# Kernel optimization log

Hardware: AMD Instinct MI355X
Metric: run time of the kernel (lower is better)

Reference implementation:

```python
import jax, jax.numpy as jnp
import numpy as np

ALPHA = 0.1
NUM_CLASSES = 10000
FEAT_DIM = 256
BATCH = 8192


def setup_inputs() -> dict:
    key = jax.random.key(0)
    k1, k2, k3 = jax.random.split(key, 3)
    feat = jax.random.normal(k1, (BATCH, FEAT_DIM), dtype=jnp.float32)
    label = jax.random.randint(k2, (BATCH,), 0, NUM_CLASSES, dtype=jnp.int64)
    # centers parameter, initialized ~ randn as in the torch constructor
    centers = jax.random.normal(k3, (NUM_CLASSES, FEAT_DIM), dtype=jnp.float32)
    return {"feat": feat, "label": label, "centers": centers}


def reference(feat, label, centers):
    B = feat.shape[0]
    # dist[b,c] = ||feat[b] - centers[c]||^2, computed in GEMM form:
    # ||f||^2 + ||c||^2 - 2 f.c  (same math as the broadcast diff^2 sum)
    f_sq = jnp.sum(feat * feat, axis=-1, keepdims=True)          # [B, 1]
    c_sq = jnp.sum(centers * centers, axis=-1)[None, :]          # [1, C]
    cross = jnp.einsum('bd,cd->bc', feat, centers)               # [B, C]
    dist = f_sq + c_sq - 2.0 * cross                             # [B, C]

    # one-hot margin scaling: y_onehot = alpha * onehot(label) + 1
    onehot = jax.nn.one_hot(label, NUM_CLASSES, dtype=dist.dtype)  # [B, C]
    margin_dist = dist * (onehot * ALPHA + 1.0)

    margin_logits = -0.5 * margin_dist
    logits = -0.5 * dist

    # likelihood: mean over batch of 0.5 * ||feat - centers[label]||^2
    cdiff = feat - centers[label]                                 # [B, D]
    likelihood = jnp.sum(cdiff * cdiff) / (2.0 * B)
    return (logits, margin_logits, likelihood)
```

## Files before the change

### kernel.cpp

```cpp
#include <hip/hip_runtime.h>
#include <hip/hip_bf16.h>


#define ALPHA_ 0.1f
constexpr int BATCH = 8192;
constexpr int NCLS  = 10000;
constexpr int FDIM  = 256;

typedef __attribute__((ext_vector_type(8))) short bf16x8;
typedef __attribute__((ext_vector_type(4))) float f32x4;

__device__ __forceinline__ unsigned short f2bf(float f) {
  unsigned int u = __float_as_uint(f);
  u += 0x7FFF + ((u >> 16) & 1);
  return (unsigned short)(u >> 16);
}

__global__ void prep_kernel(const float* __restrict__ feat,
                            const float* __restrict__ centers,
                            unsigned short* __restrict__ fbf,
                            unsigned short* __restrict__ cbf,
                            float* __restrict__ fsq,
                            float* __restrict__ csq) {
  int gw = (int)((blockIdx.x * blockDim.x + threadIdx.x) >> 6);
  int lane = threadIdx.x & 63;
  if (gw >= BATCH + NCLS) return;
  const float* src; unsigned short* dst; float* sq;
  if (gw < BATCH) {
    src = feat + (size_t)gw * FDIM; dst = fbf + (size_t)gw * FDIM; sq = fsq + gw;
  } else {
    int r = gw - BATCH;
    src = centers + (size_t)r * FDIM; dst = cbf + (size_t)r * FDIM; sq = csq + r;
  }
  float4 v = reinterpret_cast<const float4*>(src)[lane];
  ushort4 b;
  b.x = f2bf(v.x); b.y = f2bf(v.y); b.z = f2bf(v.z); b.w = f2bf(v.w);
  reinterpret_cast<ushort4*>(dst)[lane] = b;
  float s = v.x*v.x + v.y*v.y + v.z*v.z + v.w*v.w;
  #pragma unroll
  for (int off = 32; off >= 1; off >>= 1) s += __shfl_xor(s, off, 64);
  if (lane == 0) *sq = s;
}

#define BM 128
#define BN 128
#define BK 32
constexpr int NTN = 79;
constexpr int NWG = (BATCH / BM) * NTN;

__global__ __launch_bounds__(256, 4)
void gemm_kernel(const unsigned short* __restrict__ fbf,
                 const unsigned short* __restrict__ cbf,
                 const float* __restrict__ fsq,
                 const float* __restrict__ csq,
                 const int* __restrict__ label,
                 float* __restrict__ out_logits,
                 float* __restrict__ out_margin,
                 float* __restrict__ lik_row) {
  __shared__ unsigned short As[2][BM * BK];
  __shared__ unsigned short Bs[2][BN * BK];

  int bid = blockIdx.x;
  int wg = (bid & 7) * (NWG >> 3) + (bid >> 3);
  int mt = wg / NTN;
  int nt = wg - mt * NTN;

  const int tid  = threadIdx.x;
  const int lane = tid & 63;
  const int wid  = tid >> 6;
  const int wr   = (wid >> 1) * 64;
  const int wc   = (wid & 1) * 64;
  const int sr   = tid >> 1;
  const int scp  = (tid & 1) * 2;
  const int mloc  = wr + (lane & 15);
  const int nbase = wc + ((lane >> 4) << 2);
  const int ch    = lane >> 4;

  f32x4 acc[4][4];
  #pragma unroll
  for (int i = 0; i < 4; i++)
    #pragma unroll
    for (int j = 0; j < 4; j++) acc[i][j] = (f32x4){0.f, 0.f, 0.f, 0.f};

  const size_t a_base = (size_t)(mt * BM) * FDIM;
  const int c0 = nt * BN;

  bf16x8 va0, va1, vb0, vb1;
  #define LOADT(k0_) do {                                                      \
    const unsigned short* ap = fbf + a_base + (size_t)sr * FDIM + (k0_) + scp * 8; \
    va0 = *reinterpret_cast<const bf16x8*>(ap);                                \
    va1 = *reinterpret_cast<const bf16x8*>(ap + 8);                            \
    int cc = c0 + sr; cc = (cc < NCLS) ? cc : (NCLS - 1);                      \
    const unsigned short* bp = cbf + (size_t)cc * FDIM + (k0_) + scp * 8;      \
    vb0 = *reinterpret_cast<const bf16x8*>(bp);                                \
    vb1 = *reinterpret_cast<const bf16x8*>(bp + 8);                            \
  } while (0)

  #define STORET(b_) do {                                                      \
    int f_ = (sr >> 1) & 3;                                                    \
    int o0 = sr * BK + ((scp ^ f_) * 8);                                       \
    int o1 = sr * BK + (((scp + 1) ^ f_) * 8);                                 \
    *reinterpret_cast<bf16x8*>(&As[b_][o0]) = va0;                             \
    *reinterpret_cast<bf16x8*>(&As[b_][o1]) = va1;                             \
    *reinterpret_cast<bf16x8*>(&Bs[b_][o0]) = vb0;                             \
    *reinterpret_cast<bf16x8*>(&Bs[b_][o1]) = vb1;                             \
  } while (0)

  LOADT(0);
  STORET(0);

  #pragma unroll
  for (int kc = 0; kc < FDIM / BK; ++kc) {
    const int cur = kc & 1;
    if (kc < FDIM / BK - 1) LOADT((kc + 1) * BK);
    __syncthreads();
    bf16x8 a[4], b[4];
    #pragma unroll
    for (int i = 0; i < 4; i++) {
      int row = wr + i * 16 + (lane & 15);
      a[i] = *reinterpret_cast<const bf16x8*>(&As[cur][row * BK + ((ch ^ ((row >> 1) & 3)) * 8)]);
    }
    #pragma unroll
    for (int j = 0; j < 4; j++) {
      int row = wc + j * 16 + (lane & 15);
      b[j] = *reinterpret_cast<const bf16x8*>(&Bs[cur][row * BK + ((ch ^ ((row >> 1) & 3)) * 8)]);
    }
    #pragma unroll
    for (int i = 0; i < 4; i++)
      #pragma unroll
      for (int j = 0; j < 4; j++)
        acc[i][j] = __builtin_amdgcn_mfma_f32_16x16x32_bf16(b[j], a[i], acc[i][j], 0, 0, 0);
    if (kc < FDIM / BK - 1) STORET(cur ^ 1);
  }

  #pragma unroll
  for (int i = 0; i < 4; i++) {
    int m = mt * BM + mloc + i * 16;
    float fs = fsq[m];
    int lb = label[m];
    size_t rowoff = (size_t)m * NCLS;
    #pragma unroll
    for (int j = 0; j < 4; j++) {
      int n0 = c0 + nbase + j * 16;
      if (n0 >= NCLS) continue;
      float4 cs = *reinterpret_cast<const float4*>(&csq[n0]);
      f32x4 v = acc[i][j];
      f32x4 lg;
      lg[0] = v[0] - 0.5f * (fs + cs.x);
      lg[1] = v[1] - 0.5f * (fs + cs.y);
      lg[2] = v[2] - 0.5f * (fs + cs.z);
      lg[3] = v[3] - 0.5f * (fs + cs.w);
      *reinterpret_cast<f32x4*>(&out_logits[rowoff + n0]) = lg;
      f32x4 mg;
      mg[0] = (lb == n0    ) ? lg[0] * (1.0f + ALPHA_) : lg[0];
      mg[1] = (lb == n0 + 1) ? lg[1] * (1.0f + ALPHA_) : lg[1];
      mg[2] = (lb == n0 + 2) ? lg[2] * (1.0f + ALPHA_) : lg[2];
      mg[3] = (lb == n0 + 3) ? lg[3] * (1.0f + ALPHA_) : lg[3];
      *reinterpret_cast<f32x4*>(&out_margin[rowoff + n0]) = mg;
      if (lb >= n0 && lb < n0 + 4) {
        float lv = (lb == n0) ? lg[0] : (lb == n0 + 1) ? lg[1]
                 : (lb == n0 + 2) ? lg[2] : lg[3];
        lik_row[m] = -lv;
      }
    }
  }
  #undef LOADT
  #undef STORET
}

__global__ void lik_reduce_kernel(const float* __restrict__ lik_row,
                                  float* __restrict__ out) {
  int t = threadIdx.x;
  float v = 0.f;
  #pragma unroll
  for (int i = 0; i < BATCH / 1024; i++) v += lik_row[t + i * 1024];
  #pragma unroll
  for (int off = 32; off >= 1; off >>= 1) v += __shfl_xor(v, off, 64);
  __shared__ float red[16];
  if ((t & 63) == 0) red[t >> 6] = v;
  __syncthreads();
  if (t == 0) {
    float s = 0.f;
    #pragma unroll
    for (int i = 0; i < 16; i++) s += red[i];
    out[0] = s * (1.0f / BATCH);
  }
}

extern "C" void kernel_launch(void* const* d_in, const int* in_sizes, int n_in,
                              void* d_out, int out_size, void* d_ws, size_t ws_size,
                              hipStream_t stream) {
  const float* feat    = (const float*)d_in[0];
  const int*   label   = (const int*)d_in[1];
  const float* centers = (const float*)d_in[2];

  float* out        = (float*)d_out;
  float* out_logits = out;
  float* out_margin = out + (size_t)BATCH * NCLS;
  float* out_lik    = out + 2 * (size_t)BATCH * NCLS;

  char* ws = (char*)d_ws;
  unsigned short* fbf = (unsigned short*)ws;
  unsigned short* cbf = (unsigned short*)(ws + (size_t)BATCH * FDIM * 2);
  float* fsq     = (float*)(ws + (size_t)BATCH * FDIM * 2 + (size_t)NCLS * FDIM * 2);
  float* csq     = fsq + BATCH;
  float* lik_row = csq + NCLS;

  prep_kernel<<<(BATCH + NCLS) / 4, 256, 0, stream>>>(feat, centers, fbf, cbf, fsq, csq);
  gemm_kernel<<<NWG, 256, 0, stream>>>(
      fbf, cbf, fsq, csq, label, out_logits, out_margin, lik_row);
  lik_reduce_kernel<<<1, 1024, 0, stream>>>(lik_row, out_lik);
}
```

Measured before the change: 209.3 us.

## Load MFMA operands directly from global memory, dropping LDS staging

Removes the double-buffered shared-memory tiles and barriers from the GEMM. Each wave now loads its A and B fragments straight from global memory into registers for every 32-wide K step. This drops the LDS traffic and __syncthreads, and relies on L1/L2 to absorb the duplicate loads between waves that share rows. Each fragment is read by two waves, and the loads are 16-byte gathers strided by row, so cache efficiency may suffer. The kernel is already dominated by output stores.

```diff
diff --git a/kernel.cpp b/kernel.cpp
--- a/kernel.cpp
+++ b/kernel.cpp
@@ -44,7 +44,6 @@
 
 #define BM 128
 #define BN 128
-#define BK 32
 constexpr int NTN = 79;
 constexpr int NWG = (BATCH / BM) * NTN;
 
@@ -57,24 +56,31 @@
                  float* __restrict__ out_logits,
                  float* __restrict__ out_margin,
                  float* __restrict__ lik_row) {
-  __shared__ unsigned short As[2][BM * BK];
-  __shared__ unsigned short Bs[2][BN * BK];
-
   int bid = blockIdx.x;
   int wg = (bid & 7) * (NWG >> 3) + (bid >> 3);
   int mt = wg / NTN;
   int nt = wg - mt * NTN;
+  const int c0 = nt * BN;
 
   const int tid  = threadIdx.x;
   const int lane = tid & 63;
   const int wid  = tid >> 6;
   const int wr   = (wid >> 1) * 64;
   const int wc   = (wid & 1) * 64;
-  const int sr   = tid >> 1;
-  const int scp  = (tid & 1) * 2;
   const int mloc  = wr + (lane & 15);
   const int nbase = wc + ((lane >> 4) << 2);
-  const int ch    = lane >> 4;
+
+  const unsigned short* arow[4];
+  const unsigned short* brow[4];
+  #pragma unroll
+  for (int i = 0; i < 4; i++)
+    arow[i] = fbf + (size_t)(mt * BM + wr + i * 16 + (lane & 15)) * FDIM + ((lane >> 4) << 3);
+  #pragma unroll
+  for (int j = 0; j < 4; j++) {
+    int r = c0 + wc + j * 16 + (lane & 15);
+    r = (r < NCLS) ? r : (NCLS - 1);
+    brow[j] = cbf + (size_t)r * FDIM + ((lane >> 4) << 3);
+  }
 
   f32x4 acc[4][4];
   #pragma unroll
@@ -82,55 +88,20 @@
     #pragma unroll
     for (int j = 0; j < 4; j++) acc[i][j] = (f32x4){0.f, 0.f, 0.f, 0.f};
 
-  const size_t a_base = (size_t)(mt * BM) * FDIM;
-  const int c0 = nt * BN;
-
-  bf16x8 va0, va1, vb0, vb1;
-  #define LOADT(k0_) do {                                                      \
-    const unsigned short* ap = fbf + a_base + (size_t)sr * FDIM + (k0_) + scp * 8; \
-    va0 = *reinterpret_cast<const bf16x8*>(ap);                                \
-    va1 = *reinterpret_cast<const bf16x8*>(ap + 8);                            \
-    int cc = c0 + sr; cc = (cc < NCLS) ? cc : (NCLS - 1);                      \
-    const unsigned short* bp = cbf + (size_t)cc * FDIM + (k0_) + scp * 8;      \
-    vb0 = *reinterpret_cast<const bf16x8*>(bp);                                \
-    vb1 = *reinterpret_cast<const bf16x8*>(bp + 8);                            \
-  } while (0)
-
-  #define STORET(b_) do {                                                      \
-    int f_ = (sr >> 1) & 3;                                                    \
-    int o0 = sr * BK + ((scp ^ f_) * 8);                                       \
-    int o1 = sr * BK + (((scp + 1) ^ f_) * 8);                                 \
-    *reinterpret_cast<bf16x8*>(&As[b_][o0]) = va0;                             \
-    *reinterpret_cast<bf16x8*>(&As[b_][o1]) = va1;                             \
-    *reinterpret_cast<bf16x8*>(&Bs[b_][o0]) = vb0;                             \
-    *reinterpret_cast<bf16x8*>(&Bs[b_][o1]) = vb1;                             \
-  } while (0)
-
-  LOADT(0);
-  STORET(0);
-
   #pragma unroll
-  for (int kc = 0; kc < FDIM / BK; ++kc) {
-    const int cur = kc & 1;
-    if (kc < FDIM / BK - 1) LOADT((kc + 1) * BK);
-    __syncthreads();
+  for (int kk = 0; kk < FDIM / 32; ++kk) {
     bf16x8 a[4], b[4];
     #pragma unroll
-    for (int i = 0; i < 4; i++) {
-      int row = wr + i * 16 + (lane & 15);
-      a[i] = *reinterpret_cast<const bf16x8*>(&As[cur][row * BK + ((ch ^ ((row >> 1) & 3)) * 8)]);
-    }
+    for (int i = 0; i < 4; i++)
+      a[i] = *reinterpret_cast<const bf16x8*>(arow[i] + kk * 32);
     #pragma unroll
-    for (int j = 0; j < 4; j++) {
-      int row = wc + j * 16 + (lane & 15);
-      b[j] = *reinterpret_cast<const bf16x8*>(&Bs[cur][row * BK + ((ch ^ ((row >> 1) & 3)) * 8)]);
-    }
+    for (int j = 0; j < 4; j++)
+      b[j] = *reinterpret_cast<const bf16x8*>(brow[j] + kk * 32);
     #pragma unroll
     for (int i = 0; i < 4; i++)
       #pragma unroll
       for (int j = 0; j < 4; j++)
         acc[i][j] = __builtin_amdgcn_mfma_f32_16x16x32_bf16(b[j], a[i], acc[i][j], 0, 0, 0);
-    if (kc < FDIM / BK - 1) STORET(cur ^ 1);
   }
 
   #pragma unroll
@@ -164,8 +135,6 @@
       }
     }
   }
-  #undef LOADT
-  #undef STORET
 }
 
 __global__ void lik_reduce_kernel(const float* __restrict__ lik_row,
```

New measurement: 292.9 us. 1.4x slower.
